# Kernel tuning notes

Measured on AMD Instinct MI355X. Metric: run time of the kernel, lower is better.

The kernel has to match this reference:

```python
import jax, jax.numpy as jnp
import numpy as np

N_HEADS = 12
N_GROUPS = 32
EPS = 1e-5


def setup_inputs() -> dict:
    key = jax.random.key(0)
    ks = jax.random.split(key, 6)
    B, C, H, W = 8, 768, 32, 32
    EC, S = 768, 256
    x = jax.random.normal(ks[0], (B, C, H, W), dtype=jnp.float32)
    encoder_out = jax.random.normal(ks[1], (B, EC, S), dtype=jnp.float32)
    gn_w = jnp.ones((C,), jnp.float32)
    gn_b = jnp.zeros((C,), jnp.float32)
    qkv_w = jax.random.normal(ks[2], (3 * C, C), dtype=jnp.float32) * 0.02
    qkv_b = jnp.zeros((3 * C,), jnp.float32)
    enc_w = jax.random.normal(ks[3], (2 * C, EC), dtype=jnp.float32) * 0.02
    enc_b = jnp.zeros((2 * C,), jnp.float32)
    proj_w = jax.random.normal(ks[4], (C, C), dtype=jnp.float32) * 0.02
    proj_b = jnp.zeros((C,), jnp.float32)
    return {"x": x, "encoder_out": encoder_out, "gn_w": gn_w, "gn_b": gn_b,
            "qkv_w": qkv_w, "qkv_b": qkv_b, "enc_w": enc_w, "enc_b": enc_b,
            "proj_w": proj_w, "proj_b": proj_b}


def _group_norm(x, w, b):
    # x: [B, C, T]
    B, C, T = x.shape
    xg = x.reshape(B, N_GROUPS, C // N_GROUPS, T)
    mean = jnp.mean(xg, axis=(2, 3), keepdims=True)
    var = jnp.var(xg, axis=(2, 3), keepdims=True)
    xn = ((xg - mean) * jax.lax.rsqrt(var + EPS)).reshape(B, C, T)
    return xn * w[None, :, None] + b[None, :, None]


def reference(x, encoder_out, gn_w, gn_b, qkv_w, qkv_b, enc_w, enc_b, proj_w, proj_b):
    B, C, Hs, Ws = x.shape
    T = Hs * Ws
    ch = C // N_HEADS
    xf = x.reshape(B, C, T)
    xn = _group_norm(xf, gn_w, gn_b)
    # 1x1 conv == channel matmul
    qkv = jnp.einsum('oc,bct->bot', qkv_w, xn) + qkv_b[None, :, None]  # [B, 3C, T]
    # torch layout: per-head contiguous blocks of [q, k, v]
    qkv = qkv.reshape(B * N_HEADS, 3 * ch, T)
    q, k, v = qkv[:, :ch], qkv[:, ch:2 * ch], qkv[:, 2 * ch:]
    ekv = jnp.einsum('oc,bcs->bos', enc_w, encoder_out) + enc_b[None, :, None]  # [B, 2C, S]
    ekv = ekv.reshape(B * N_HEADS, 2 * ch, -1)
    ek, ev = ekv[:, :ch], ekv[:, ch:]
    k = jnp.concatenate([ek, k], axis=-1)  # [BH, ch, S+T]
    v = jnp.concatenate([ev, v], axis=-1)
    scale = 1.0 / np.sqrt(np.sqrt(ch))
    w = jnp.einsum('bct,bcs->bts', q * scale, k * scale)  # [BH, T, S+T]
    w = jax.nn.softmax(w.astype(jnp.float32), axis=-1).astype(q.dtype)
    a = jnp.einsum('bts,bcs->bct', w, v).reshape(B, C, T)
    h = jnp.einsum('oc,bct->bot', proj_w, a) + proj_b[None, :, None]
    return (xf + h).reshape(B, C, Hs, Ws)
```

## Files before the change

### kernel.cpp

```cpp
#include <hip/hip_runtime.h>

typedef __attribute__((ext_vector_type(8))) short bf16x8;
typedef __attribute__((ext_vector_type(4))) float f32x4;
typedef __attribute__((ext_vector_type(16))) float f32x16;
typedef __attribute__((ext_vector_type(4))) float float4v;
typedef __attribute__((ext_vector_type(4))) unsigned short ushort4v;
typedef __attribute__((ext_vector_type(8))) unsigned short ushort8v;

#define DEVINL __device__ __forceinline__


DEVINL unsigned short f2bf(float f) {
  union { float f; unsigned u; } v; v.f = f;
  unsigned r = (v.u + 0x7fffu + ((v.u >> 16) & 1u)) >> 16;
  return (unsigned short)r;
}
DEVINL unsigned short f2bfr(float f) {
  union { float f; unsigned u; } v; v.f = f;
  return (unsigned short)((v.u + 0x8000u) >> 16);
}
DEVINL float bf2f(unsigned short h) {
  union { unsigned u; float f; } v; v.u = ((unsigned)h) << 16;
  return v.f;
}
DEVINL float exp2a(float x) {
#if __has_builtin(__builtin_amdgcn_exp2f)
  return __builtin_amdgcn_exp2f(x);
#else
  float r; asm("v_exp_f32 %0, %1" : "=v"(r) : "v"(x)); return r;
#endif
}
DEVINL void gload16(const void* g, void* l) {
  __builtin_amdgcn_global_load_lds(
      (const __attribute__((address_space(1))) unsigned*)g,
      (__attribute__((address_space(3))) unsigned*)l, 16, 0, 0);
}
DEVINL bf16x8 mkfrag(unsigned a, unsigned b, unsigned c, unsigned d) {
  union { unsigned u[4]; bf16x8 v; } x;
  x.u[0] = a; x.u[1] = b; x.u[2] = c; x.u[3] = d;
  return x.v;
}

__global__ __launch_bounds__(256) void k_cvt(const float* __restrict__ s,
                                             unsigned short* __restrict__ d, int n4) {
  int i = blockIdx.x * 256 + threadIdx.x;
  if (i >= n4) return;
  float4v v = *(const float4v*)(s + (size_t)i * 4);
  ushort4v o;
  o[0] = f2bf(v[0]); o[1] = f2bf(v[1]); o[2] = f2bf(v[2]); o[3] = f2bf(v[3]);
  *(ushort4v*)(d + (size_t)i * 4) = o;
}

__global__ __launch_bounds__(256) void k_gn(const float* __restrict__ x,
                                            const float* __restrict__ gw,
                                            const float* __restrict__ gb,
                                            unsigned short* __restrict__ xnt) {
  int g = blockIdx.x, b = blockIdx.y, tid = threadIdx.x;
  const float* xb = x + ((size_t)b * 768 + g * 24) * 1024;
  float s = 0.f, ss = 0.f;
  for (int i = tid; i < 6144; i += 256) {
    float4v v = *(const float4v*)(xb + (size_t)i * 4);
    s += v[0] + v[1] + v[2] + v[3];
    ss += v[0] * v[0] + v[1] * v[1] + v[2] * v[2] + v[3] * v[3];
  }
  #pragma unroll
  for (int o = 32; o > 0; o >>= 1) { s += __shfl_down(s, o); ss += __shfl_down(ss, o); }
  __shared__ float rs[4], rss[4], stat[2];
  int w = tid >> 6;
  if ((tid & 63) == 0) { rs[w] = s; rss[w] = ss; }
  __syncthreads();
  if (tid == 0) {
    float S = rs[0] + rs[1] + rs[2] + rs[3], SS = rss[0] + rss[1] + rss[2] + rss[3];
    float mean = S / 24576.f;
    float var = SS / 24576.f - mean * mean;
    stat[0] = mean; stat[1] = rsqrtf(fmaxf(var, 0.f) + 1e-5f);
  }
  __syncthreads();
  float mean = stat[0], rstd = stat[1];
  float wv[24], bv[24];
  #pragma unroll
  for (int c = 0; c < 24; ++c) { wv[c] = gw[g * 24 + c]; bv[c] = gb[g * 24 + c]; }
  for (int it = 0; it < 4; ++it) {
    int t = it * 256 + tid;
    ushort8v ov[3];
    #pragma unroll
    for (int c = 0; c < 24; ++c) {
      float v = xb[(size_t)c * 1024 + t];
      ov[c >> 3][c & 7] = f2bf((v - mean) * rstd * wv[c] + bv[c]);
    }
    ushort8v* dst = (ushort8v*)(xnt + ((size_t)(b * 1024 + t)) * 768 + g * 24);
    dst[0] = ov[0]; dst[1] = ov[1]; dst[2] = ov[2];
  }
}

__global__ __launch_bounds__(256) void k_enc_tr(const float* __restrict__ enc,
                                                unsigned short* __restrict__ et) {
  int ct = blockIdx.x * 64, st = blockIdx.y * 64, b = blockIdx.z, tid = threadIdx.x;
  __shared__ unsigned short L[64 * 72];
  #pragma unroll
  for (int it = 0; it < 4; ++it) {
    int idx = it * 256 + tid; int r = idx >> 4, ch = idx & 15;
    float4v v = *(const float4v*)(enc + ((size_t)(b * 768 + ct + r)) * 256 + st + ch * 4);
    ushort4v o;
    o[0] = f2bf(v[0]); o[1] = f2bf(v[1]); o[2] = f2bf(v[2]); o[3] = f2bf(v[3]);
    *(ushort4v*)&L[r * 72 + ch * 4] = o;
  }
  __syncthreads();
  #pragma unroll
  for (int it = 0; it < 2; ++it) {
    int idx = it * 256 + tid; int s = idx >> 3, ch = idx & 7;
    ushort8v o;
    #pragma unroll
    for (int j = 0; j < 8; ++j) o[j] = L[(ch * 8 + j) * 72 + s];
    *(ushort8v*)(et + ((size_t)(b * 256 + st + s)) * 768 + ct + ch * 8) = o;
  }
}

__global__ __launch_bounds__(256) void k_vcat(const unsigned short* __restrict__ qkvt,
                                              const unsigned short* __restrict__ ekvt,
                                              unsigned short* __restrict__ vcat) {
  int s0 = blockIdx.x * 64, bh = blockIdx.y, b = bh / 12, h = bh % 12, tid = threadIdx.x;
  __shared__ unsigned short L[64 * 72];
  #pragma unroll
  for (int it = 0; it < 2; ++it) {
    int idx = it * 256 + tid; int s = idx >> 3, ch = idx & 7;
    int sg = s0 + s;
    const unsigned short* src = (sg < 256)
        ? ekvt + ((size_t)(b * 256 + sg)) * 1536 + h * 128 + 64 + ch * 8
        : qkvt + ((size_t)(b * 1024 + sg - 256)) * 2304 + h * 192 + 128 + ch * 8;
    *(ushort8v*)&L[s * 72 + ch * 8] = *(const ushort8v*)src;
  }
  __syncthreads();
  #pragma unroll
  for (int it = 0; it < 2; ++it) {
    int idx = it * 256 + tid; int c = idx >> 3, ch = idx & 7;
    ushort8v o;
    #pragma unroll
    for (int j = 0; j < 8; ++j) o[j] = L[(ch * 8 + j) * 72 + c];
    *(ushort8v*)(vcat + ((size_t)bh * 64 + c) * 1280 + s0 + ch * 8) = o;
  }
}

template <int EPI>
__global__ __launch_bounds__(256) void k_gemm(const unsigned short* __restrict__ A,
                                              const unsigned short* __restrict__ B,
                                              const float* __restrict__ bias,
                                              const float* __restrict__ resid,
                                              void* __restrict__ outp,
                                              int N, int K,
                                              long sA, long sB, long sO, long sR) {
  int bz = blockIdx.z;
  int m0 = blockIdx.x * 128, n0 = blockIdx.y * 128;
  const unsigned short* Ab = A + (size_t)bz * sA + (size_t)m0 * K;
  const unsigned short* Bb = B + (size_t)bz * sB + (size_t)n0 * K;
  __shared__ unsigned short As[128 * 32], Bs[128 * 32];
  int tid = threadIdx.x, lane = tid & 63, w = tid >> 6;
  int ln = lane & 15, lg = lane >> 4;
  int wm = (w >> 1) * 64, wn = (w & 1) * 64;
  int sr = lane >> 2, sc = lane & 3;
  int rA0 = w * 16 + sr, rA1 = w * 16 + 64 + sr;
  const unsigned short* ga0 = Ab + (size_t)rA0 * K + ((sc ^ (rA0 & 3)) * 8);
  const unsigned short* ga1 = Ab + (size_t)rA1 * K + ((sc ^ (rA1 & 3)) * 8);
  const unsigned short* gb0 = Bb + (size_t)rA0 * K + ((sc ^ (rA0 & 3)) * 8);
  const unsigned short* gb1 = Bb + (size_t)rA1 * K + ((sc ^ (rA1 & 3)) * 8);
  unsigned short* la0 = &As[(w * 16) * 32];
  unsigned short* la1 = &As[(w * 16 + 64) * 32];
  unsigned short* lb0 = &Bs[(w * 16) * 32];
  unsigned short* lb1 = &Bs[(w * 16 + 64) * 32];
  int swz = (lg ^ (ln & 3)) * 8;

  f32x4 acc[4][4];
  #pragma unroll
  for (int i = 0; i < 4; ++i)
    #pragma unroll
    for (int j = 0; j < 4; ++j) acc[i][j] = (f32x4){0.f, 0.f, 0.f, 0.f};

  for (int k0 = 0; k0 < K; k0 += 32) {
    gload16(ga0 + k0, la0);
    gload16(ga1 + k0, la1);
    gload16(gb0 + k0, lb0);
    gload16(gb1 + k0, lb1);
    __syncthreads();
    bf16x8 af[4], bfv[4];
    #pragma unroll
    for (int i = 0; i < 4; ++i) af[i] = *(const bf16x8*)&As[(wm + i * 16 + ln) * 32 + swz];
    #pragma unroll
    for (int i = 0; i < 4; ++i) bfv[i] = *(const bf16x8*)&Bs[(wn + i * 16 + ln) * 32 + swz];
    #pragma unroll
    for (int i = 0; i < 4; ++i)
      #pragma unroll
      for (int j = 0; j < 4; ++j)
        acc[i][j] = __builtin_amdgcn_mfma_f32_16x16x32_bf16(af[i], bfv[j], acc[i][j], 0, 0, 0);
    __syncthreads();
  }

  #pragma unroll
  for (int i = 0; i < 4; ++i) {
    #pragma unroll
    for (int j = 0; j < 4; ++j) {
      #pragma unroll
      for (int r = 0; r < 4; ++r) {
        int row = m0 + wm + i * 16 + lg * 4 + r;
        int col = n0 + wn + j * 16 + ln;
        float v = acc[i][j][r];
        if (EPI == 0) {
          v += bias[col];
          ((unsigned short*)outp)[(size_t)bz * sO + (size_t)row * N + col] = f2bf(v);
        } else {
          v += bias[row] + resid[(size_t)bz * sR + (size_t)row * N + col];
          ((float*)outp)[(size_t)bz * sO + (size_t)row * N + col] = v;
        }
      }
    }
  }
}

__global__ __launch_bounds__(256, 3) void k_attn(const unsigned short* __restrict__ qkvt,
                                                 const unsigned short* __restrict__ ekvt,
                                                 const unsigned short* __restrict__ vcat,
                                                 unsigned short* __restrict__ at) {
  int bid = blockIdx.x;
  int swb = (bid & 7) * 96 + (bid >> 3);
  int t0 = (swb & 7) * 128, bh = swb >> 3, b = bh / 12, h = bh % 12;
  int tid = threadIdx.x, w = tid >> 6, lane = tid & 63;
  int ql = lane & 31, hi = lane >> 5;
  __shared__ unsigned short Ks[2][64 * 64], Vs[2][64 * 64];

  const float QSC = 0.125f * 1.44269504089f;
  bf16x8 aq[4];
  const unsigned short* qrow = qkvt + ((size_t)(b * 1024 + t0 + w * 32 + ql)) * 2304 + h * 192;
  #pragma unroll
  for (int jc = 0; jc < 4; ++jc) {
    ushort8v qv = *(const ushort8v*)(qrow + jc * 16 + hi * 8);
    bf16x8 o;
    #pragma unroll
    for (int e = 0; e < 8; ++e) o[e] = (short)f2bf(bf2f(qv[e]) * QSC);
    aq[jc] = o;
  }

  int r0 = tid >> 3, r1 = r0 + 32, ch16 = (tid & 7) * 16;
  int wr0 = r0 * 128 + (ch16 ^ ((r0 & 7) << 4));
  int wr1 = r1 * 128 + (ch16 ^ ((r0 & 7) << 4));
  const unsigned short* ke = ekvt + ((size_t)b * 256) * 1536 + h * 128 + (tid & 7) * 8;
  const unsigned short* kq = qkvt + ((long)(b * 1024) - 256) * 2304 + h * 192 + 64 + (tid & 7) * 8;
  const unsigned short* vb = vcat + ((size_t)bh * 64) * 1280 + (tid & 7) * 8;

  {
    ushort8v k0 = *(const ushort8v*)(ke + (size_t)r0 * 1536);
    ushort8v k1 = *(const ushort8v*)(ke + (size_t)r1 * 1536);
    ushort8v v0 = *(const ushort8v*)(vb + (size_t)r0 * 1280);
    ushort8v v1 = *(const ushort8v*)(vb + (size_t)r1 * 1280);
    *(ushort8v*)((char*)&Ks[0][0] + wr0) = k0;
    *(ushort8v*)((char*)&Ks[0][0] + wr1) = k1;
    *(ushort8v*)((char*)&Vs[0][0] + wr0) = v0;
    *(ushort8v*)((char*)&Vs[0][0] + wr1) = v1;
  }
  __syncthreads();

  f32x16 acc0, acc1;
  #pragma unroll
  for (int r = 0; r < 16; ++r) { acc0[r] = 0.f; acc1[r] = 0.f; }
  float m = -1e30f, l = 0.f;
  int xp = (ql & 7) << 4;

  for (int t = 0; t < 20; ++t) {
    int cur = t & 1, nxt = cur ^ 1;
    ushort8v kr0, kr1, vr0, vr1;
    if (t < 19) {
      int sg0 = (t + 1) * 64 + r0, sg1 = sg0 + 32;
      kr0 = (t + 1 < 4) ? *(const ushort8v*)(ke + (size_t)sg0 * 1536)
                        : *(const ushort8v*)(kq + (size_t)sg0 * 2304);
      kr1 = (t + 1 < 4) ? *(const ushort8v*)(ke + (size_t)sg1 * 1536)
                        : *(const ushort8v*)(kq + (size_t)sg1 * 2304);
      vr0 = *(const ushort8v*)(vb + (size_t)r0 * 1280 + (t + 1) * 64);
      vr1 = *(const ushort8v*)(vb + (size_t)r1 * 1280 + (t + 1) * 64);
    }
    f32x16 sf0, sf1;
    #pragma unroll
    for (int r = 0; r < 16; ++r) { sf0[r] = 0.f; sf1[r] = 0.f; }
    const char* kbase = (const char*)&Ks[cur][0] + ql * 128;
    __builtin_amdgcn_s_setprio(1);
    #pragma unroll
    for (int jc = 0; jc < 4; ++jc) {
      int off = (jc * 32 + hi * 16) ^ xp;
      bf16x8 k0f = *(const bf16x8*)(kbase + off);
      bf16x8 k1f = *(const bf16x8*)(kbase + 4096 + off);
      sf0 = __builtin_amdgcn_mfma_f32_32x32x16_bf16(k0f, aq[jc], sf0, 0, 0, 0);
      sf1 = __builtin_amdgcn_mfma_f32_32x32x16_bf16(k1f, aq[jc], sf1, 0, 0, 0);
    }
    __builtin_amdgcn_s_setprio(0);

    float mx[8];
    #pragma unroll
    for (int i = 0; i < 8; ++i)
      mx[i] = fmaxf(fmaxf(sf0[i], sf0[i + 8]), fmaxf(sf1[i], sf1[i + 8]));
    #pragma unroll
    for (int o = 4; o > 0; o >>= 1)
      #pragma unroll
      for (int i = 0; i < 4; ++i)
        if (i < o) mx[i] = fmaxf(mx[i], mx[i + o]);
    float mt = fmaxf(mx[0], __shfl_xor(mx[0], 32));
    if (!__all(mt <= m + 8.f)) {
      float mn = fmaxf(m, mt);
      float al = exp2a(m - mn);
      l *= al;
      #pragma unroll
      for (int r = 0; r < 16; ++r) { acc0[r] *= al; acc1[r] *= al; }
      m = mn;
    }

    const char* vbase = (const char*)&Vs[cur][0] + ql * 128;
    #pragma unroll
    for (int sb = 0; sb < 2; ++sb) {
      unsigned pk[8];
      #pragma unroll
      for (int i = 0; i < 8; ++i) {
        float pa = exp2a((sb ? sf1[2 * i] : sf0[2 * i]) - m);
        float pb = exp2a((sb ? sf1[2 * i + 1] : sf0[2 * i + 1]) - m);
        l += pa + pb;
        pk[i] = (unsigned)f2bfr(pa) | ((unsigned)f2bfr(pb) << 16);
      }
      unsigned E1 = __shfl_xor(hi ? pk[0] : pk[2], 32);
      unsigned E2 = __shfl_xor(hi ? pk[1] : pk[3], 32);
      unsigned E3 = __shfl_xor(hi ? pk[4] : pk[6], 32);
      unsigned E4 = __shfl_xor(hi ? pk[5] : pk[7], 32);
      bf16x8 fj0 = hi ? mkfrag(E1, E2, pk[2], pk[3]) : mkfrag(pk[0], pk[1], E1, E2);
      bf16x8 fj1 = hi ? mkfrag(E3, E4, pk[6], pk[7]) : mkfrag(pk[4], pk[5], E3, E4);
      __builtin_amdgcn_s_setprio(1);
      #pragma unroll
      for (int jj = 0; jj < 2; ++jj) {
        int off = (sb * 64 + jj * 32 + hi * 16) ^ xp;
        bf16x8 v0f = *(const bf16x8*)(vbase + off);
        bf16x8 v1f = *(const bf16x8*)(vbase + 4096 + off);
        bf16x8 pf = jj ? fj1 : fj0;
        acc0 = __builtin_amdgcn_mfma_f32_32x32x16_bf16(v0f, pf, acc0, 0, 0, 0);
        acc1 = __builtin_amdgcn_mfma_f32_32x32x16_bf16(v1f, pf, acc1, 0, 0, 0);
      }
      __builtin_amdgcn_s_setprio(0);
    }

    if (t < 19) {
      *(ushort8v*)((char*)&Ks[nxt][0] + wr0) = kr0;
      *(ushort8v*)((char*)&Ks[nxt][0] + wr1) = kr1;
      *(ushort8v*)((char*)&Vs[nxt][0] + wr0) = vr0;
      *(ushort8v*)((char*)&Vs[nxt][0] + wr1) = vr1;
    }
    __syncthreads();
  }

  l += __shfl_xor(l, 32);
  float rl = 1.f / l;
  unsigned short* orow = at + ((size_t)(b * 1024 + t0 + w * 32 + ql)) * 768 + h * 64;
  #pragma unroll
  for (int cb = 0; cb < 2; ++cb) {
    #pragma unroll
    for (int g = 0; g < 4; ++g) {
      int c = cb * 32 + g * 8 + hi * 4;
      ushort4v o;
      #pragma unroll
      for (int i = 0; i < 4; ++i) {
        float v = (cb ? acc1[g * 4 + i] : acc0[g * 4 + i]) * rl;
        o[i] = f2bf(v);
      }
      *(ushort4v*)(orow + c) = o;
    }
  }
}

extern "C" void kernel_launch(void* const* d_in, const int* in_sizes, int n_in,
                              void* d_out, int out_size, void* d_ws, size_t ws_size,
                              hipStream_t stream) {
  const float* x      = (const float*)d_in[0];
  const float* enc    = (const float*)d_in[1];
  const float* gn_w   = (const float*)d_in[2];
  const float* gn_b   = (const float*)d_in[3];
  const float* qkv_w  = (const float*)d_in[4];
  const float* qkv_b  = (const float*)d_in[5];
  const float* enc_w  = (const float*)d_in[6];
  const float* enc_b  = (const float*)d_in[7];
  const float* proj_w = (const float*)d_in[8];
  const float* proj_b = (const float*)d_in[9];
  float* out = (float*)d_out;

  char* ws = (char*)d_ws;
  unsigned short* w_qkv = (unsigned short*)(ws + 0);
  unsigned short* w_enc = (unsigned short*)(ws + 3538944);
  unsigned short* w_prj = (unsigned short*)(ws + 5898240);
  unsigned short* xn_t  = (unsigned short*)(ws + 7077888);
  unsigned short* enc_t = (unsigned short*)(ws + 19660800);
  unsigned short* qkv_t = (unsigned short*)(ws + 22806528);
  unsigned short* ekv_t = (unsigned short*)(ws + 60555264);
  unsigned short* vcat  = (unsigned short*)(ws + 66846720);
  unsigned short* a_t   = xn_t;

  k_cvt<<<1728, 256, 0, stream>>>(qkv_w, w_qkv, 442368);
  k_cvt<<<1152, 256, 0, stream>>>(enc_w, w_enc, 294912);
  k_cvt<<<576, 256, 0, stream>>>(proj_w, w_prj, 147456);
  k_gn<<<dim3(32, 8), 256, 0, stream>>>(x, gn_w, gn_b, xn_t);
  k_enc_tr<<<dim3(12, 4, 8), 256, 0, stream>>>(enc, enc_t);
  k_gemm<0><<<dim3(8, 18, 8), 256, 0, stream>>>(xn_t, w_qkv, qkv_b, nullptr, qkv_t,
                                                2304, 768, 786432L, 0L, 2359296L, 0L);
  k_gemm<0><<<dim3(2, 12, 8), 256, 0, stream>>>(enc_t, w_enc, enc_b, nullptr, ekv_t,
                                                1536, 768, 196608L, 0L, 393216L, 0L);
  k_vcat<<<dim3(20, 96), 256, 0, stream>>>(qkv_t, ekv_t, vcat);
  k_attn<<<dim3(768), 256, 0, stream>>>(qkv_t, ekv_t, vcat, a_t);
  k_gemm<1><<<dim3(6, 8, 8), 256, 0, stream>>>(w_prj, a_t, proj_b, x, out,
                                               1024, 768, 0L, 786432L, 786432L, 786432L);
}
```

Measured before the change: 193.4 us.

## Stage attention K/V tiles with direct global-to-LDS loads and permlane32 swap

The attention kernel now stages K and V tiles with global_load_lds DMA straight into shared memory instead of loading into registers and storing to LDS. The swizzle moves from the LDS write address to a per-lane choice of source column. The four cross-half shuffles used to build the P fragment become v_permlane32_swap instructions. This is meant to cut register pressure, VGPR-to-LDS store traffic and ds_bpermute cost, at the price of an explicit vmcnt wait before each barrier.

After: 192.6 us. No clear change (-0.4%).

```diff
diff --git a/kernel.cpp b/kernel.cpp
--- a/kernel.cpp
+++ b/kernel.cpp
@@ -34,6 +34,9 @@
   __builtin_amdgcn_global_load_lds(
       (const __attribute__((address_space(1))) unsigned*)g,
       (__attribute__((address_space(3))) unsigned*)l, 16, 0, 0);
+}
+DEVINL void plswap(unsigned& a, unsigned& b) {
+  asm("v_permlane32_swap_b32 %0, %1" : "+v"(a), "+v"(b));
 }
 DEVINL bf16x8 mkfrag(unsigned a, unsigned b, unsigned c, unsigned d) {
   union { unsigned u[4]; bf16x8 v; } x;
@@ -224,7 +227,7 @@
   int t0 = (swb & 7) * 128, bh = swb >> 3, b = bh / 12, h = bh % 12;
   int tid = threadIdx.x, w = tid >> 6, lane = tid & 63;
   int ql = lane & 31, hi = lane >> 5;
-  __shared__ unsigned short Ks[2][64 * 64], Vs[2][64 * 64];
+  __shared__ unsigned short Ks[2][4096], Vs[2][4096];
 
   const float QSC = 0.125f * 1.44269504089f;
   bf16x8 aq[4];
@@ -238,23 +241,30 @@
     aq[jc] = o;
   }
 
-  int r0 = tid >> 3, r1 = r0 + 32, ch16 = (tid & 7) * 16;
-  int wr0 = r0 * 128 + (ch16 ^ ((r0 & 7) << 4));
-  int wr1 = r1 * 128 + (ch16 ^ ((r0 & 7) << 4));
-  const unsigned short* ke = ekvt + ((size_t)b * 256) * 1536 + h * 128 + (tid & 7) * 8;
-  const unsigned short* kq = qkvt + ((long)(b * 1024) - 256) * 2304 + h * 192 + 64 + (tid & 7) * 8;
-  const unsigned short* vb = vcat + ((size_t)bh * 64) * 1280 + (tid & 7) * 8;
-
-  {
-    ushort8v k0 = *(const ushort8v*)(ke + (size_t)r0 * 1536);
-    ushort8v k1 = *(const ushort8v*)(ke + (size_t)r1 * 1536);
-    ushort8v v0 = *(const ushort8v*)(vb + (size_t)r0 * 1280);
-    ushort8v v1 = *(const ushort8v*)(vb + (size_t)r1 * 1280);
-    *(ushort8v*)((char*)&Ks[0][0] + wr0) = k0;
-    *(ushort8v*)((char*)&Ks[0][0] + wr1) = k1;
-    *(ushort8v*)((char*)&Vs[0][0] + wr0) = v0;
-    *(ushort8v*)((char*)&Vs[0][0] + wr1) = v1;
-  }
+  int rloc = w * 16 + (lane >> 3);
+  int chunk = (lane & 7) ^ (lane >> 3);
+  const unsigned short* ke_st = ekvt + ((size_t)(b * 256 + rloc)) * 1536 + h * 128 + chunk * 8;
+  const unsigned short* kq_st = qkvt + ((long)b * 1024 - 256 + rloc) * 2304 + h * 192 + 64 + chunk * 8;
+  const unsigned short* v_st  = vcat + ((size_t)(bh * 64 + rloc)) * 1280 + chunk * 8;
+  unsigned short* kd = &Ks[0][0] + w * 1024;
+  unsigned short* vd = &Vs[0][0] + w * 1024;
+
+  auto stage = [&](int nb, int tn) {
+    const unsigned short* ks;
+    size_t rstep;
+    if (tn < 4) { ks = ke_st + (size_t)tn * 64 * 1536; rstep = 8 * 1536; }
+    else        { ks = kq_st + (size_t)tn * 64 * 2304; rstep = 8 * 2304; }
+    unsigned short* kdd = kd + nb * 4096;
+    unsigned short* vdd = vd + nb * 4096;
+    const unsigned short* vs = v_st + tn * 64;
+    gload16(ks, kdd);
+    gload16(ks + rstep, kdd + 512);
+    gload16(vs, vdd);
+    gload16(vs + 8 * 1280, vdd + 512);
+  };
+
+  stage(0, 0);
+  asm volatile("s_waitcnt vmcnt(0)" ::: "memory");
   __syncthreads();
 
   f32x16 acc0, acc1;
@@ -264,17 +274,9 @@
   int xp = (ql & 7) << 4;
 
   for (int t = 0; t < 20; ++t) {
-    int cur = t & 1, nxt = cur ^ 1;
-    ushort8v kr0, kr1, vr0, vr1;
-    if (t < 19) {
-      int sg0 = (t + 1) * 64 + r0, sg1 = sg0 + 32;
-      kr0 = (t + 1 < 4) ? *(const ushort8v*)(ke + (size_t)sg0 * 1536)
-                        : *(const ushort8v*)(kq + (size_t)sg0 * 2304);
-      kr1 = (t + 1 < 4) ? *(const ushort8v*)(ke + (size_t)sg1 * 1536)
-                        : *(const ushort8v*)(kq + (size_t)sg1 * 2304);
-      vr0 = *(const ushort8v*)(vb + (size_t)r0 * 1280 + (t + 1) * 64);
-      vr1 = *(const ushort8v*)(vb + (size_t)r1 * 1280 + (t + 1) * 64);
-    }
+    int cur = t & 1;
+    if (t < 19) stage(cur ^ 1, t + 1);
+
     f32x16 sf0, sf1;
     #pragma unroll
     for (int r = 0; r < 16; ++r) { sf0[r] = 0.f; sf1[r] = 0.f; }
@@ -320,12 +322,12 @@
         l += pa + pb;
         pk[i] = (unsigned)f2bfr(pa) | ((unsigned)f2bfr(pb) << 16);
       }
-      unsigned E1 = __shfl_xor(hi ? pk[0] : pk[2], 32);
-      unsigned E2 = __shfl_xor(hi ? pk[1] : pk[3], 32);
-      unsigned E3 = __shfl_xor(hi ? pk[4] : pk[6], 32);
-      unsigned E4 = __shfl_xor(hi ? pk[5] : pk[7], 32);
-      bf16x8 fj0 = hi ? mkfrag(E1, E2, pk[2], pk[3]) : mkfrag(pk[0], pk[1], E1, E2);
-      bf16x8 fj1 = hi ? mkfrag(E3, E4, pk[6], pk[7]) : mkfrag(pk[4], pk[5], E3, E4);
+      plswap(pk[0], pk[2]);
+      plswap(pk[1], pk[3]);
+      plswap(pk[4], pk[6]);
+      plswap(pk[5], pk[7]);
+      bf16x8 fj0 = mkfrag(pk[0], pk[1], pk[2], pk[3]);
+      bf16x8 fj1 = mkfrag(pk[4], pk[5], pk[6], pk[7]);
       __builtin_amdgcn_s_setprio(1);
       #pragma unroll
       for (int jj = 0; jj < 2; ++jj) {
@@ -339,12 +341,7 @@
       __builtin_amdgcn_s_setprio(0);
     }
 
-    if (t < 19) {
-      *(ushort8v*)((char*)&Ks[nxt][0] + wr0) = kr0;
-      *(ushort8v*)((char*)&Ks[nxt][0] + wr1) = kr1;
-      *(ushort8v*)((char*)&Vs[nxt][0] + wr0) = vr0;
-      *(ushort8v*)((char*)&Vs[nxt][0] + wr1) = vr1;
-    }
+    if (t < 19) asm volatile("s_waitcnt vmcnt(0)" ::: "memory");
     __syncthreads();
   }
 
```
